# Kernel tuning notes

Hardware: AMD Instinct MI355X
Metric: run time of the kernel (lower is better)

## Reference

```python
import jax, jax.numpy as jnp
import numpy as np

B, K, V, N, M, TOPK = 256, 256, 256, 4000, 4000, 8
EPS = 1e-8  # torch F.cosine_similarity default eps


def setup_inputs() -> dict:
    key = jax.random.key(0)
    ks = jax.random.split(key, 6)
    query_key = jax.random.normal(ks[0], (B, K), dtype=jnp.float32)
    W_k = jax.random.normal(ks[1], (K, K), dtype=jnp.float32) / np.sqrt(K).astype(np.float32)
    b_k = jnp.zeros((K,), dtype=jnp.float32)
    assoc_matrix = jax.random.normal(ks[2], (N, K, V), dtype=jnp.float32) * 0.02
    usage_counter = jax.random.uniform(ks[3], (N,), dtype=jnp.float32) * 10.0
    memory_index = jax.random.randint(ks[4], (M,), 0, N)
    return {
        "query_key": query_key,
        "W_k": W_k,
        "b_k": b_k,
        "assoc_matrix": assoc_matrix,
        "usage_counter": usage_counter,
        "memory_index": memory_index,
        "top_k": TOPK,
    }


def reference(query_key, W_k, b_k, assoc_matrix, usage_counter, memory_index, top_k):
    # key_encoder: Linear + Tanh
    e = jnp.tanh(query_key @ W_k.T + b_k)                      # [B, K]
    # stored keys = first value-column of each used slot (irregular gather)
    stored_keys = assoc_matrix[memory_index, :, 0]             # [M, K]
    # cosine similarity (vectorized form of the per-slot python loop)
    qn = e / jnp.maximum(jnp.linalg.norm(e, axis=-1, keepdims=True), EPS)
    kn = stored_keys / jnp.maximum(jnp.linalg.norm(stored_keys, axis=-1, keepdims=True), EPS)
    sims = qn @ kn.T                                           # [B, M]
    top_sims, top_idx = jax.lax.top_k(sims, top_k)             # [B, k]
    actual = memory_index[top_idx]                             # [B, k] slot ids
    # confidence = sim * (1 + log(1 + usage))
    confidences = top_sims * (1.0 + jnp.log1p(usage_counter[actual]))
    # gather stored associations and retrieve values: e @ A[actual]
    gathered = assoc_matrix[actual]                            # [B, k, K, V]
    retrieved_values = jnp.einsum('bd,bkdv->bkv', e, gathered) # [B, k, V]
    return retrieved_values, confidences, top_sims
```

## Files before the change

### kernel.cpp

```cpp
#include <hip/hip_runtime.h>
#include <math.h>

#define BB 256
#define KK 256
#define VV 256
#define MM 4000
#define TOPK 8

__global__ void k_proj(const float* __restrict__ qk, const float* __restrict__ Wk,
                       const float* __restrict__ bk, double* __restrict__ e64,
                       double* __restrict__ qn64) {
    int b = blockIdx.x, j = threadIdx.x;
    __shared__ float q[KK];
    __shared__ double red[256];
    q[j] = qk[b * KK + j];
    __syncthreads();
    const float* w = Wk + (size_t)j * KK;
    double acc = 0.0;
#pragma unroll 4
    for (int d = 0; d < KK; ++d) acc += (double)q[d] * (double)w[d];
    double val = tanh(acc + (double)bk[j]);
    e64[b * KK + j] = val;
    red[j] = val * val;
    __syncthreads();
    for (int s = 128; s > 0; s >>= 1) {
        if (j < s) red[j] += red[j + s];
        __syncthreads();
    }
    double nrm = fmax(sqrt(red[0]), 1e-8);
    qn64[b * KK + j] = val / nrm;
}

__global__ void k_kn(const float* __restrict__ A, const int* __restrict__ midx,
                     double* __restrict__ kn64) {
    int m = blockIdx.x, t = threadIdx.x;
    size_t n = (size_t)midx[m];
    double val = (double)A[n * (size_t)(KK * VV) + (size_t)t * VV];
    __shared__ double red[256];
    red[t] = val * val;
    __syncthreads();
    for (int s = 128; s > 0; s >>= 1) {
        if (t < s) red[t] += red[t + s];
        __syncthreads();
    }
    double nrm = fmax(sqrt(red[0]), 1e-8);
    kn64[(size_t)m * KK + t] = val / nrm;
}

#define BMS 16
#define BNS 64
#define KS  16
__global__ void __launch_bounds__(64) k_sims(
        const double* __restrict__ qn, const double* __restrict__ kn,
        double* __restrict__ sims) {
    __shared__ double qsT[2][KS][BMS + 2];
    __shared__ double ksT[2][KS][BNS + 8];
    int tid = threadIdx.x;
    int tx = tid & 15, ty = tid >> 4;
    int m0 = blockIdx.x * BNS, b0 = blockIdx.y * BMS;
    int qr = tid & 15;
    int qc = (tid >> 4) * 4;
    int krr = tid >> 3;
    int kc = (tid & 7) * 2;
    const double* qrow = qn + (size_t)(b0 + qr) * KK;
    double acc[4][4] = {};
    int pb = tx * 4 + (tx >> 2) * 2;

    {
        double qreg[4]; double2 kreg[8]; int rr[8];
#pragma unroll
        for (int j = 0; j < 4; ++j) qreg[j] = qrow[qc + j];
#pragma unroll
        for (int s = 0; s < 8; ++s) {
            int r = krr + s * 8; rr[s] = r;
            int mrow = m0 + r;
            const double* kp = kn + (size_t)(mrow < MM ? mrow : 0) * KK + kc;
            kreg[s] = (mrow < MM) ? *(const double2*)kp : make_double2(0.0, 0.0);
        }
#pragma unroll
        for (int j = 0; j < 4; ++j) qsT[0][qc + j][qr] = qreg[j];
#pragma unroll
        for (int s = 0; s < 8; ++s) {
            int p = rr[s] + (rr[s] >> 4) * 2;
            ksT[0][kc][p]     = kreg[s].x;
            ksT[0][kc + 1][p] = kreg[s].y;
        }
    }
    __syncthreads();

    for (int t = 0; t < KK / KS; ++t) {
        int cur = t & 1;
        double qreg[4]; double2 kreg[8]; int rr[8];
        bool have = (t < KK / KS - 1);
        if (have) {
            int kk2 = (t + 1) * KS;
#pragma unroll
            for (int j = 0; j < 4; ++j) qreg[j] = qrow[kk2 + qc + j];
#pragma unroll
            for (int s = 0; s < 8; ++s) {
                int r = krr + s * 8; rr[s] = r;
                int mrow = m0 + r;
                const double* kp = kn + (size_t)(mrow < MM ? mrow : 0) * KK + kk2 + kc;
                kreg[s] = (mrow < MM) ? *(const double2*)kp : make_double2(0.0, 0.0);
            }
        }
#pragma unroll
        for (int i = 0; i < KS; ++i) {
            double qv[4], kv[4];
            *(double2*)&qv[0] = *(const double2*)&qsT[cur][i][ty * 4];
            *(double2*)&qv[2] = *(const double2*)&qsT[cur][i][ty * 4 + 2];
            *(double2*)&kv[0] = *(const double2*)&ksT[cur][i][pb];
            *(double2*)&kv[2] = *(const double2*)&ksT[cur][i][pb + 2];
#pragma unroll
            for (int a = 0; a < 4; ++a)
#pragma unroll
                for (int c = 0; c < 4; ++c)
                    acc[a][c] += qv[a] * kv[c];
        }
        if (have) {
            int nxt = cur ^ 1;
#pragma unroll
            for (int j = 0; j < 4; ++j) qsT[nxt][qc + j][qr] = qreg[j];
#pragma unroll
            for (int s = 0; s < 8; ++s) {
                int p = rr[s] + (rr[s] >> 4) * 2;
                ksT[nxt][kc][p]     = kreg[s].x;
                ksT[nxt][kc + 1][p] = kreg[s].y;
            }
        }
        __syncthreads();
    }
#pragma unroll
    for (int a = 0; a < 4; ++a) {
        int bb = b0 + ty * 4 + a;
#pragma unroll
        for (int c = 0; c < 4; ++c) {
            int mm2 = m0 + tx * 4 + c;
            if (mm2 < MM) sims[(size_t)bb * MM + mm2] = acc[a][c];
        }
    }
}

__global__ void k_topk(const double* __restrict__ sims, const int* __restrict__ midx,
                       const float* __restrict__ usage, float* __restrict__ out_conf,
                       float* __restrict__ out_sims, int* __restrict__ acts) {
    int b = blockIdx.x, t = threadIdx.x;
    double v[TOPK];
    int id[TOPK];
#pragma unroll
    for (int i = 0; i < TOPK; ++i) { v[i] = -INFINITY; id[i] = 0x7fffffff; }
    const double* row = sims + (size_t)b * MM;
    for (int m = t; m < MM; m += 256) {
        double x = row[m];
        if (x > v[TOPK - 1]) {
            v[TOPK - 1] = x; id[TOPK - 1] = m;
#pragma unroll
            for (int i = TOPK - 1; i > 0; --i) {
                if (v[i] > v[i - 1]) {
                    double tv = v[i]; v[i] = v[i - 1]; v[i - 1] = tv;
                    int ti = id[i]; id[i] = id[i - 1]; id[i - 1] = ti;
                }
            }
        }
    }
    __shared__ double sv[256 * TOPK];
    __shared__ int si[256 * TOPK];
#pragma unroll
    for (int i = 0; i < TOPK; ++i) { sv[t * TOPK + i] = v[i]; si[t * TOPK + i] = id[i]; }
    __syncthreads();
    for (int stride = 128; stride > 0; stride >>= 1) {
        if (t < stride) {
            double* av = &sv[t * TOPK];
            int*    ai = &si[t * TOPK];
            double* bv = &sv[(t + stride) * TOPK];
            int*    bi = &si[(t + stride) * TOPK];
            double mv[TOPK]; int mi[TOPK];
            int pa = 0, pb = 0;
#pragma unroll
            for (int i = 0; i < TOPK; ++i) {
                double va = av[pa], vb = bv[pb];
                bool takeA = (va > vb) || (va == vb && ai[pa] < bi[pb]);
                if (takeA) { mv[i] = va; mi[i] = ai[pa]; ++pa; }
                else       { mv[i] = vb; mi[i] = bi[pb]; ++pb; }
            }
#pragma unroll
            for (int i = 0; i < TOPK; ++i) { av[i] = mv[i]; ai[i] = mi[i]; }
        }
        __syncthreads();
    }
    if (t < TOPK) {
        double val = sv[t];
        int idx = si[t];
        int actual = midx[idx];
        out_sims[b * TOPK + t] = (float)val;
        out_conf[b * TOPK + t] = (float)(val * (1.0 + log1p((double)usage[actual])));
        acts[b * TOPK + t] = actual;
    }
}

__global__ void __launch_bounds__(256) k_retr(
        const float* __restrict__ A, const double* __restrict__ e64,
        const int* __restrict__ acts, float* __restrict__ out) {
    int bk_ = blockIdx.x;
    int b = bk_ >> 3;
    int tid = threadIdx.x;
    int w = tid >> 6, l = tid & 63;
    size_t n = (size_t)acts[bk_];
    const float* Ap = A + n * (size_t)(KK * VV);
    __shared__ float es[KK];
    __shared__ float part[4][64][4];
    es[tid] = (float)e64[b * KK + tid];
    __syncthreads();
    float ax = 0.f, ay = 0.f, az = 0.f, aw = 0.f;
    const float* base = Ap + (size_t)(w * 64) * VV + 4 * l;
#pragma unroll 8
    for (int dd = 0; dd < 64; ++dd) {
        float ev = es[w * 64 + dd];
        const float4 a = *reinterpret_cast<const float4*>(base + (size_t)dd * VV);
        ax = fmaf(ev, a.x, ax); ay = fmaf(ev, a.y, ay);
        az = fmaf(ev, a.z, az); aw = fmaf(ev, a.w, aw);
    }
    part[w][l][0] = ax; part[w][l][1] = ay; part[w][l][2] = az; part[w][l][3] = aw;
    __syncthreads();
    int l2 = tid >> 2, j = tid & 3;
    float s = part[0][l2][j] + part[1][l2][j] + part[2][l2][j] + part[3][l2][j];
    out[(size_t)bk_ * VV + tid] = s;
}

extern "C" void kernel_launch(void* const* d_in, const int* in_sizes, int n_in,
                              void* d_out, int out_size, void* d_ws, size_t ws_size,
                              hipStream_t stream) {
    const float* qk    = (const float*)d_in[0];
    const float* Wk    = (const float*)d_in[1];
    const float* bk    = (const float*)d_in[2];
    const float* A     = (const float*)d_in[3];
    const float* usage = (const float*)d_in[4];
    const int*   midx  = (const int*)d_in[5];

    float* out   = (float*)d_out;
    float* retr  = out;
    float* conf  = out + (size_t)BB * TOPK * VV;
    float* tsims = conf + BB * TOPK;

    double* ws64  = (double*)d_ws;
    double* e64   = ws64;
    double* qn64  = e64 + BB * KK;
    double* kn64  = qn64 + BB * KK;
    double* sims  = kn64 + (size_t)MM * KK;
    int*    acts  = (int*)(sims + (size_t)BB * MM);

    k_proj<<<BB, 256, 0, stream>>>(qk, Wk, bk, e64, qn64);
    k_kn<<<MM, 256, 0, stream>>>(A, midx, kn64);
    dim3 g3((MM + BNS - 1) / BNS, BB / BMS);
    k_sims<<<g3, 64, 0, stream>>>(qn64, kn64, sims);
    k_topk<<<BB, 256, 0, stream>>>(sims, midx, usage, conf, tsims, acts);
    k_retr<<<BB * TOPK, 256, 0, stream>>>(A, e64, acts, retr);
}
```

Baseline: 174.3 us.

## Deduplicate retrieval by slot so each gathered matrix is read once

Adds an ownership pass in which atomicMin picks one block per distinct slot id among the top-k results. The owning block collects every (b,k) pair that maps to that slot and computes their outputs, two at a time, while streaming the 256KB association matrix. Other blocks exit early. This cuts redundant HBM reads when queries share slots, at the cost of two extra launches, a serial loop per block and possible load imbalance on popular slots.

```diff
diff --git a/kernel.cpp b/kernel.cpp
--- a/kernel.cpp
+++ b/kernel.cpp
@@ -4,6 +4,7 @@
 #define BB 256
 #define KK 256
 #define VV 256
+#define NN 4000
 #define MM 4000
 #define TOPK 8
 
@@ -198,33 +199,73 @@
     }
 }
 
+__global__ void __launch_bounds__(256) k_own_init(int* __restrict__ own) {
+    int i = blockIdx.x * 256 + threadIdx.x;
+    if (i < NN) own[i] = 0x7fffffff;
+}
+__global__ void __launch_bounds__(256) k_own_min(const int* __restrict__ acts,
+                                                 int* __restrict__ own) {
+    int i = blockIdx.x * 256 + threadIdx.x;
+    atomicMin(&own[acts[i]], i);
+}
+
 __global__ void __launch_bounds__(256) k_retr(
         const float* __restrict__ A, const double* __restrict__ e64,
-        const int* __restrict__ acts, float* __restrict__ out) {
+        const int* __restrict__ acts, const int* __restrict__ own,
+        float* __restrict__ out) {
     int bk_ = blockIdx.x;
-    int b = bk_ >> 3;
+    int n_i = acts[bk_];
+    if (own[n_i] != bk_) return;
+
+    __shared__ int list[BB * TOPK];
+    __shared__ int cnt_s;
+    __shared__ float es[2][KK];
+    __shared__ float part[2][4][64][4];
     int tid = threadIdx.x;
+    if (tid == 0) cnt_s = 0;
+    __syncthreads();
+    for (int j = tid; j < BB * TOPK; j += 256)
+        if (acts[j] == n_i) list[atomicAdd(&cnt_s, 1)] = j;
+    __syncthreads();
+    int cn = cnt_s;
+
     int w = tid >> 6, l = tid & 63;
-    size_t n = (size_t)acts[bk_];
-    const float* Ap = A + n * (size_t)(KK * VV);
-    __shared__ float es[KK];
-    __shared__ float part[4][64][4];
-    es[tid] = (float)e64[b * KK + tid];
-    __syncthreads();
-    float ax = 0.f, ay = 0.f, az = 0.f, aw = 0.f;
-    const float* base = Ap + (size_t)(w * 64) * VV + 4 * l;
+    const float* base = A + (size_t)n_i * (KK * VV) + (size_t)(w * 64) * VV + 4 * l;
+
+    for (int c0 = 0; c0 < cn; c0 += 2) {
+        int s0 = list[c0];
+        int s1 = (c0 + 1 < cn) ? list[c0 + 1] : -1;
+        es[0][tid] = (float)e64[(s0 >> 3) * KK + tid];
+        es[1][tid] = (s1 >= 0) ? (float)e64[(s1 >> 3) * KK + tid] : 0.f;
+        __syncthreads();
+        float ax0 = 0.f, ay0 = 0.f, az0 = 0.f, aw0 = 0.f;
+        float ax1 = 0.f, ay1 = 0.f, az1 = 0.f, aw1 = 0.f;
 #pragma unroll 8
-    for (int dd = 0; dd < 64; ++dd) {
-        float ev = es[w * 64 + dd];
-        const float4 a = *reinterpret_cast<const float4*>(base + (size_t)dd * VV);
-        ax = fmaf(ev, a.x, ax); ay = fmaf(ev, a.y, ay);
-        az = fmaf(ev, a.z, az); aw = fmaf(ev, a.w, aw);
-    }
-    part[w][l][0] = ax; part[w][l][1] = ay; part[w][l][2] = az; part[w][l][3] = aw;
-    __syncthreads();
-    int l2 = tid >> 2, j = tid & 3;
-    float s = part[0][l2][j] + part[1][l2][j] + part[2][l2][j] + part[3][l2][j];
-    out[(size_t)bk_ * VV + tid] = s;
+        for (int dd = 0; dd < 64; ++dd) {
+            const float4 a = *reinterpret_cast<const float4*>(base + (size_t)dd * VV);
+            float e0 = es[0][w * 64 + dd];
+            ax0 = fmaf(e0, a.x, ax0); ay0 = fmaf(e0, a.y, ay0);
+            az0 = fmaf(e0, a.z, az0); aw0 = fmaf(e0, a.w, aw0);
+            float e1 = es[1][w * 64 + dd];
+            ax1 = fmaf(e1, a.x, ax1); ay1 = fmaf(e1, a.y, ay1);
+            az1 = fmaf(e1, a.z, az1); aw1 = fmaf(e1, a.w, aw1);
+        }
+        part[0][w][l][0] = ax0; part[0][w][l][1] = ay0;
+        part[0][w][l][2] = az0; part[0][w][l][3] = aw0;
+        part[1][w][l][0] = ax1; part[1][w][l][1] = ay1;
+        part[1][w][l][2] = az1; part[1][w][l][3] = aw1;
+        __syncthreads();
+        int l2 = tid >> 2, j = tid & 3;
+        float r0 = part[0][0][l2][j] + part[0][1][l2][j]
+                 + part[0][2][l2][j] + part[0][3][l2][j];
+        out[(size_t)s0 * VV + tid] = r0;
+        if (s1 >= 0) {
+            float r1 = part[1][0][l2][j] + part[1][1][l2][j]
+                     + part[1][2][l2][j] + part[1][3][l2][j];
+            out[(size_t)s1 * VV + tid] = r1;
+        }
+        __syncthreads();
+    }
 }
 
 extern "C" void kernel_launch(void* const* d_in, const int* in_sizes, int n_in,
@@ -248,11 +289,14 @@
     double* kn64  = qn64 + BB * KK;
     double* sims  = kn64 + (size_t)MM * KK;
     int*    acts  = (int*)(sims + (size_t)BB * MM);
+    int*    own   = acts + BB * TOPK;
 
     k_proj<<<BB, 256, 0, stream>>>(qk, Wk, bk, e64, qn64);
     k_kn<<<MM, 256, 0, stream>>>(A, midx, kn64);
+    k_own_init<<<(NN + 255) / 256, 256, 0, stream>>>(own);
     dim3 g3((MM + BNS - 1) / BNS, BB / BMS);
     k_sims<<<g3, 64, 0, stream>>>(qn64, kn64, sims);
     k_topk<<<BB, 256, 0, stream>>>(sims, midx, usage, conf, tsims, acts);
-    k_retr<<<BB * TOPK, 256, 0, stream>>>(A, e64, acts, retr);
-}
+    k_own_min<<<(BB * TOPK) / 256, 256, 0, stream>>>(acts, own);
+    k_retr<<<BB * TOPK, 256, 0, stream>>>(A, e64, acts, own, retr);
+}
```

Result: no change. 175.7 us (+0.8%).

## Shrink sims tile to 8 rows and use row-major padded LDS layout

Applied to the files above, without the earlier changes.

The fp64 similarity GEMM tile drops from 16x64 to 8x64 rows per block, so each thread computes a 2x4 micro-tile instead of 4x4 and the grid has twice as many blocks. Shared tiles change from transposed padded arrays to row-major arrays with a stride of 17 to avoid bank conflicts, and each thread now handles strided columns (tx+16c). The aim is more parallelism and simpler conflict-free LDS stores. The cost is lower register reuse per LDS load, scalar rather than vectorized LDS reads, and non-contiguous output writes.

```diff
diff --git a/kernel.cpp b/kernel.cpp
--- a/kernel.cpp
+++ b/kernel.cpp
@@ -47,29 +47,28 @@
     kn64[(size_t)m * KK + t] = val / nrm;
 }
 
-#define BMS 16
+#define BMS 8
 #define BNS 64
 #define KS  16
+#define LSTR 17
 __global__ void __launch_bounds__(64) k_sims(
         const double* __restrict__ qn, const double* __restrict__ kn,
         double* __restrict__ sims) {
-    __shared__ double qsT[2][KS][BMS + 2];
-    __shared__ double ksT[2][KS][BNS + 8];
+    __shared__ double qs[2][BMS][LSTR];
+    __shared__ double ks[2][BNS][LSTR];
     int tid = threadIdx.x;
     int tx = tid & 15, ty = tid >> 4;
     int m0 = blockIdx.x * BNS, b0 = blockIdx.y * BMS;
-    int qr = tid & 15;
-    int qc = (tid >> 4) * 4;
+    int qr  = tid >> 3;
+    int qc2 = (tid & 7) * 2;
     int krr = tid >> 3;
-    int kc = (tid & 7) * 2;
+    int kc  = (tid & 7) * 2;
     const double* qrow = qn + (size_t)(b0 + qr) * KK;
-    double acc[4][4] = {};
-    int pb = tx * 4 + (tx >> 2) * 2;
+    double acc[2][4] = {};
 
     {
-        double qreg[4]; double2 kreg[8]; int rr[8];
-#pragma unroll
-        for (int j = 0; j < 4; ++j) qreg[j] = qrow[qc + j];
+        double2 qreg; double2 kreg[8]; int rr[8];
+        qreg = *(const double2*)(qrow + qc2);
 #pragma unroll
         for (int s = 0; s < 8; ++s) {
             int r = krr + s * 8; rr[s] = r;
@@ -77,25 +76,23 @@
             const double* kp = kn + (size_t)(mrow < MM ? mrow : 0) * KK + kc;
             kreg[s] = (mrow < MM) ? *(const double2*)kp : make_double2(0.0, 0.0);
         }
-#pragma unroll
-        for (int j = 0; j < 4; ++j) qsT[0][qc + j][qr] = qreg[j];
+        qs[0][qr][qc2]     = qreg.x;
+        qs[0][qr][qc2 + 1] = qreg.y;
 #pragma unroll
         for (int s = 0; s < 8; ++s) {
-            int p = rr[s] + (rr[s] >> 4) * 2;
-            ksT[0][kc][p]     = kreg[s].x;
-            ksT[0][kc + 1][p] = kreg[s].y;
+            ks[0][rr[s]][kc]     = kreg[s].x;
+            ks[0][rr[s]][kc + 1] = kreg[s].y;
         }
     }
     __syncthreads();
 
     for (int t = 0; t < KK / KS; ++t) {
         int cur = t & 1;
-        double qreg[4]; double2 kreg[8]; int rr[8];
+        double2 qreg; double2 kreg[8]; int rr[8];
         bool have = (t < KK / KS - 1);
         if (have) {
             int kk2 = (t + 1) * KS;
-#pragma unroll
-            for (int j = 0; j < 4; ++j) qreg[j] = qrow[kk2 + qc + j];
+            qreg = *(const double2*)(qrow + kk2 + qc2);
 #pragma unroll
             for (int s = 0; s < 8; ++s) {
                 int r = krr + s * 8; rr[s] = r;
@@ -106,36 +103,35 @@
         }
 #pragma unroll
         for (int i = 0; i < KS; ++i) {
-            double qv[4], kv[4];
-            *(double2*)&qv[0] = *(const double2*)&qsT[cur][i][ty * 4];
-            *(double2*)&qv[2] = *(const double2*)&qsT[cur][i][ty * 4 + 2];
-            *(double2*)&kv[0] = *(const double2*)&ksT[cur][i][pb];
-            *(double2*)&kv[2] = *(const double2*)&ksT[cur][i][pb + 2];
-#pragma unroll
-            for (int a = 0; a < 4; ++a)
+            double qv[2], kv[4];
+#pragma unroll
+            for (int a = 0; a < 2; ++a) qv[a] = qs[cur][ty * 2 + a][i];
+#pragma unroll
+            for (int c = 0; c < 4; ++c) kv[c] = ks[cur][tx + 16 * c][i];
+#pragma unroll
+            for (int a = 0; a < 2; ++a)
 #pragma unroll
                 for (int c = 0; c < 4; ++c)
                     acc[a][c] += qv[a] * kv[c];
         }
         if (have) {
             int nxt = cur ^ 1;
-#pragma unroll
-            for (int j = 0; j < 4; ++j) qsT[nxt][qc + j][qr] = qreg[j];
+            qs[nxt][qr][qc2]     = qreg.x;
+            qs[nxt][qr][qc2 + 1] = qreg.y;
 #pragma unroll
             for (int s = 0; s < 8; ++s) {
-                int p = rr[s] + (rr[s] >> 4) * 2;
-                ksT[nxt][kc][p]     = kreg[s].x;
-                ksT[nxt][kc + 1][p] = kreg[s].y;
-            }
-        }
-        __syncthreads();
-    }
-#pragma unroll
-    for (int a = 0; a < 4; ++a) {
-        int bb = b0 + ty * 4 + a;
+                ks[nxt][rr[s]][kc]     = kreg[s].x;
+                ks[nxt][rr[s]][kc + 1] = kreg[s].y;
+            }
+        }
+        __syncthreads();
+    }
+#pragma unroll
+    for (int a = 0; a < 2; ++a) {
+        int bb = b0 + ty * 2 + a;
 #pragma unroll
         for (int c = 0; c < 4; ++c) {
-            int mm2 = m0 + tx * 4 + c;
+            int mm2 = m0 + tx + 16 * c;
             if (mm2 < MM) sims[(size_t)bb * MM + mm2] = acc[a][c];
         }
     }
```

Measured after the change: 171.6 us. No clear change (-1.6%).
